# Kernel tuning notes

Hardware: AMD Instinct MI355X
Metric: run time of the kernel (lower is better)

Reference implementation:

```python
import jax, jax.numpy as jnp
import numpy as np

B, K, D = 262144, 100, 384
MOMENTUM = 0.95
EPS = 1e-8  # matches F.cosine_similarity eps clamp


def setup_inputs() -> dict:
    key = jax.random.key(0)
    k1, k2 = jax.random.split(key)
    embeddings = jax.random.normal(k1, (B, D), dtype=jnp.float32)
    centroids = jax.random.normal(k2, (K, D), dtype=jnp.float32)
    counts = jnp.zeros((K,), dtype=jnp.float32)
    return {"embeddings": embeddings, "centroids": centroids, "counts": counts}


def reference(embeddings, centroids, counts):
    # Batched version of compute_novelty: cosine similarity of each embedding
    # against every active cluster centroid (all K treated as active).
    e = embeddings / jnp.maximum(jnp.linalg.norm(embeddings, axis=-1, keepdims=True), EPS)
    c = centroids / jnp.maximum(jnp.linalg.norm(centroids, axis=-1, keepdims=True), EPS)
    sims = jnp.einsum('bd,kd->bk', e, c)            # [B, K] cosine similarities
    max_sim = jnp.max(sims, axis=-1)                # [B]
    closest = jnp.argmax(sims, axis=-1)             # [B] int
    novelty = 1.0 - max_sim * max_sim               # squared-distance novelty (FIX 4)

    # Batched EMA centroid update (update_cluster fused over the batch):
    # each cluster moves toward the mean of the embeddings assigned to it.
    num_k = centroids.shape[0]
    seg_sum = jax.ops.segment_sum(embeddings, closest, num_segments=num_k)   # [K, D]
    seg_cnt = jax.ops.segment_sum(jnp.ones((embeddings.shape[0],), embeddings.dtype),
                                  closest, num_segments=num_k)               # [K]
    seg_mean = seg_sum / jnp.maximum(seg_cnt, 1.0)[:, None]
    hit = (seg_cnt > 0)[:, None]
    new_centroids = jnp.where(hit, MOMENTUM * centroids + (1.0 - MOMENTUM) * seg_mean,
                              centroids)
    new_counts = counts + seg_cnt
    return novelty, closest, new_centroids, new_counts
```

## Files before the change

### kernel.cpp

```cpp
#include <hip/hip_runtime.h>
#include <math.h>

#define B_N 262144
#define K_N 100
#define D_N 384
#define EPS 1e-8f
#define MOM 0.95f
#define FLAG_THR 5e-4f
#define NBLK 256
#define ROWS_PB (B_N / NBLK)
#define KSTR 101
#define PART_N (K_N * D_N)

typedef __attribute__((ext_vector_type(8))) short short8;
typedef __attribute__((ext_vector_type(4))) float f32x4;

#define OFF_CPK   0
#define OFF_NC64  86016
#define OFF_CNT   86816
#define OFF_FLAGN 87264
#define OFF_FLAGS 87328
#define OFF_PARTS 1135904

#define GLOAD_LDS(g, l) __builtin_amdgcn_global_load_lds( \
    (const __attribute__((address_space(1))) unsigned int*)(g), \
    (__attribute__((address_space(3))) unsigned int*)(l), 16, 0, 0)

__device__ __forceinline__ size_t cpk_idx(int col, int d) {
    int kk = d >> 5, r = d & 31, lg = r >> 3, j = r & 7;
    int nt = col >> 4, l15 = col & 15;
    return (size_t)((kk * 7 + nt) * 512) + lg * 128 + l15 * 8 + j;
}

__device__ __forceinline__ unsigned short bf16_rne(float x) {
    unsigned u = __float_as_uint(x);
    unsigned r = (u + 0x7fff + ((u >> 16) & 1)) >> 16;
    return (unsigned short)r;
}

__global__ void k_norm_c(const float* __restrict__ c, unsigned short* __restrict__ cpk,
                         double* __restrict__ nc64, int* __restrict__ cnt,
                         int* __restrict__ flagn) {
    int col = blockIdx.x;
    int t = threadIdx.x;
    if (col == 112) {
        if (t < K_N) cnt[t] = 0;
        if (t == 0) *flagn = 0;
        return;
    }
    if (col >= K_N) {
        for (int d = t; d < D_N; d += 128) cpk[cpk_idx(col, d)] = 0;
        return;
    }
    const float* row = c + (size_t)col * D_N;
    double ss = 0.0;
    for (int d = t; d < D_N; d += 128) { double v = row[d]; ss += v * v; }
    __shared__ double red[2];
    for (int o = 32; o > 0; o >>= 1) ss += __shfl_down(ss, o);
    if ((t & 63) == 0) red[t >> 6] = ss;
    __syncthreads();
    double nc = fmax(sqrt(red[0] + red[1]), (double)EPS);
    if (t == 0) nc64[col] = nc;
    float inv = (float)(1.0 / nc);
    for (int d = t; d < D_N; d += 128)
        cpk[cpk_idx(col, d)] = bf16_rne(row[d] * inv);
}

__device__ __forceinline__ void splitA(float4 x0, float4 x1,
                                       short8& ah, short8& al, float& ss) {
    float xs[8] = {x0.x, x0.y, x0.z, x0.w, x1.x, x1.y, x1.z, x1.w};
#pragma unroll
    for (int j = 0; j < 8; j++) {
        float x = xs[j];
        unsigned xb = __float_as_uint(x);
        unsigned hb = xb & 0xffff0000u;
        float lf = x - __uint_as_float(hb);
        ah[j] = (short)(hb >> 16);
        al[j] = (short)bf16_rne(lf);
        ss = fmaf(x, x, ss);
    }
}

__global__ __launch_bounds__(512) void k_main(
    const float* __restrict__ e, const unsigned short* __restrict__ cpk,
    float* __restrict__ out_nov, float* __restrict__ out_cls,
    unsigned* __restrict__ flags, int* __restrict__ flagn) {
    __shared__ unsigned short sB[84 * 512];
    const int t = threadIdx.x;
    const int lane = t & 63;
    const int wid = t >> 6;
    const int l15 = lane & 15;
    const int lg = lane >> 4;
    const int rowbase = blockIdx.x * 128 + wid * 16;

    for (int c = wid; c < 84; c += 8)
        GLOAD_LDS((const char*)cpk + c * 1024 + lane * 16,
                  (char*)sB + c * 1024);

    const float* a0p = e + (size_t)(rowbase + l15) * D_N + lg * 8;

    float4 a[12][2];
#pragma unroll
    for (int kk = 0; kk < 12; kk++) {
        a[kk][0] = *(const float4*)(a0p + kk * 32);
        a[kk][1] = *(const float4*)(a0p + kk * 32 + 4);
    }

    f32x4 acc[7];
#pragma unroll
    for (int nt = 0; nt < 7; nt++) acc[nt] = f32x4{0.f, 0.f, 0.f, 0.f};
    float ss0 = 0.f;

    __syncthreads();

#pragma unroll
    for (int kk = 0; kk < 12; kk++) {
        short8 ah0, al0;
        splitA(a[kk][0], a[kk][1], ah0, al0, ss0);
#pragma unroll
        for (int nt = 0; nt < 7; nt++) {
            short8 bh = *(const short8*)(sB + (kk * 7 + nt) * 512 + lane * 8);
            acc[nt] = __builtin_amdgcn_mfma_f32_16x16x32_bf16(ah0, bh, acc[nt], 0, 0, 0);
            acc[nt] = __builtin_amdgcn_mfma_f32_16x16x32_bf16(al0, bh, acc[nt], 0, 0, 0);
        }
    }

    ss0 += __shfl_xor(ss0, 16); ss0 += __shfl_xor(ss0, 32);
    const int rl = lg * 4 + (l15 & 3);
    float ssr0 = __shfl(ss0, rl);

    float b0 = -3e38f, b1 = -3e38f, b2 = -3e38f, b3 = -3e38f;
    float s0 = -3e38f, s1 = -3e38f, s2 = -3e38f, s3 = -3e38f;
    int i0 = 0, i1 = 0, i2 = 0, i3 = 0, j0 = 0, j1 = 0, j2 = 0, j3 = 0;
#pragma unroll
    for (int nt = 0; nt < 7; nt++) {
        int cl = nt * 16 + l15;
        bool valid = cl < K_N;
        float v;
        v = valid ? acc[nt][0] : -3e38f;
        if (v > b0) { s0 = b0; j0 = i0; b0 = v; i0 = cl; } else if (v > s0) { s0 = v; j0 = cl; }
        v = valid ? acc[nt][1] : -3e38f;
        if (v > b1) { s1 = b1; j1 = i1; b1 = v; i1 = cl; } else if (v > s1) { s1 = v; j1 = cl; }
        v = valid ? acc[nt][2] : -3e38f;
        if (v > b2) { s2 = b2; j2 = i2; b2 = v; i2 = cl; } else if (v > s2) { s2 = v; j2 = cl; }
        v = valid ? acc[nt][3] : -3e38f;
        if (v > b3) { s3 = b3; j3 = i3; b3 = v; i3 = cl; } else if (v > s3) { s3 = v; j3 = cl; }
    }
#pragma unroll
    for (int w = 1; w <= 8; w <<= 1) {
#define MRG(B, S, I, J)                                                        \
        {                                                                      \
            float ob = __shfl_xor(B, w), os = __shfl_xor(S, w);                \
            int obi = __shfl_xor(I, w), osi = __shfl_xor(J, w);                \
            if (ob > B) {                                                      \
                float ns; int nsi;                                             \
                if (B > os) { ns = B; nsi = I; } else { ns = os; nsi = osi; }  \
                B = ob; I = obi; S = ns; J = nsi;                              \
            } else if (ob > S) { S = ob; J = obi; }                            \
        }
        MRG(b0, s0, i0, j0) MRG(b1, s1, i1, j1) MRG(b2, s2, i2, j2) MRG(b3, s3, i3, j3)
#undef MRG
    }
    if (l15 < 4) {
        float bb = (l15 & 2) ? ((l15 & 1) ? b3 : b2) : ((l15 & 1) ? b1 : b0);
        float sv = (l15 & 2) ? ((l15 & 1) ? s3 : s2) : ((l15 & 1) ? s1 : s0);
        int bi   = (l15 & 2) ? ((l15 & 1) ? i3 : i2) : ((l15 & 1) ? i1 : i0);
        int si   = (l15 & 2) ? ((l15 & 1) ? j3 : j2) : ((l15 & 1) ? j1 : j0);
        int grow = rowbase + rl;
        float nrm = fmaxf(sqrtf(ssr0), EPS);
        float msim = bb / nrm;
        out_nov[grow] = 1.f - msim * msim;
        out_cls[grow] = (float)bi;
        if (bb - sv < FLAG_THR * nrm) {
            int pos = atomicAdd(flagn, 1);
            flags[pos] = ((unsigned)grow << 14) | ((unsigned)bi << 7) | (unsigned)si;
        }
    }
}

__global__ void k_refine(const float* __restrict__ e, const float* __restrict__ c_raw,
                         const double* __restrict__ nc64, const int* __restrict__ flagn,
                         const unsigned* __restrict__ flags,
                         float* __restrict__ out_nov, float* __restrict__ out_cls) {
    int n = *flagn;
    int gw = (blockIdx.x * 256 + threadIdx.x) >> 6;
    int lane = threadIdx.x & 63;
    int nw = (gridDim.x * 256) >> 6;
    for (int i = gw; i < n; i += nw) {
        unsigned f = flags[i];
        int row = f >> 14, bi = (f >> 7) & 127, si = f & 127;
        const float* er = e + (size_t)row * D_N;
        const float* ca = c_raw + (size_t)bi * D_N;
        const float* cb = c_raw + (size_t)si * D_N;
        double d1 = 0, d2 = 0, ee = 0;
#pragma unroll
        for (int j = 0; j < 6; j++) {
            int d = lane * 6 + j;
            double ev = er[d];
            d1 += ev * (double)ca[d];
            d2 += ev * (double)cb[d];
            ee += ev * ev;
        }
#pragma unroll
        for (int w = 1; w <= 32; w <<= 1) {
            d1 += __shfl_xor(d1, w); d2 += __shfl_xor(d2, w); ee += __shfl_xor(ee, w);
        }
        if (lane == 0) {
            double v1 = d1 / nc64[bi], v2 = d2 / nc64[si];
            int k; double v;
            if (v2 > v1 || (v2 == v1 && si < bi)) { k = si; v = v2; } else { k = bi; v = v1; }
            double nrm = fmax(sqrt(ee), (double)EPS);
            double ms = v / nrm;
            out_nov[row] = (float)(1.0 - ms * ms);
            out_cls[row] = (float)k;
        }
    }
}

__global__ __launch_bounds__(768) void k_accum(
    const float* __restrict__ e, const float* __restrict__ cls,
    int* __restrict__ parts, int* __restrict__ cnt) {
    __shared__ int sums[D_N * KSTR];
    __shared__ int scls[ROWS_PB];
    __shared__ int h[K_N];
    const int t = threadIdx.x;
    const int rg = t / D_N;
    const int d = t - rg * D_N;
    const size_t rbase = (size_t)blockIdx.x * ROWS_PB;

    for (int i = t; i < D_N * KSTR; i += 768) sums[i] = 0;
    if (t < K_N) h[t] = 0;
    __syncthreads();
    for (int i = t; i < ROWS_PB; i += 768) {
        int k = (int)cls[rbase + i];
        scls[i] = k;
        atomicAdd(&h[k], 1);
    }
    __syncthreads();
    if (t < K_N && h[t] > 0) atomicAdd(&cnt[t], h[t]);

    const float* eb = e + rbase * D_N;
    for (int g = 0; g < ROWS_PB; g += 16) {
        const int r0 = g + rg,      r1 = g + rg + 2,  r2 = g + rg + 4,  r3 = g + rg + 6;
        const int r4 = g + rg + 8,  r5 = g + rg + 10, r6 = g + rg + 12, r7 = g + rg + 14;
        float v0 = eb[(size_t)r0 * D_N + d]; float v1 = eb[(size_t)r1 * D_N + d];
        float v2 = eb[(size_t)r2 * D_N + d]; float v3 = eb[(size_t)r3 * D_N + d];
        float v4 = eb[(size_t)r4 * D_N + d]; float v5 = eb[(size_t)r5 * D_N + d];
        float v6 = eb[(size_t)r6 * D_N + d]; float v7 = eb[(size_t)r7 * D_N + d];
        atomicAdd(&sums[d * KSTR + scls[r0]], __float2int_rn(v0 * 65536.f));
        atomicAdd(&sums[d * KSTR + scls[r1]], __float2int_rn(v1 * 65536.f));
        atomicAdd(&sums[d * KSTR + scls[r2]], __float2int_rn(v2 * 65536.f));
        atomicAdd(&sums[d * KSTR + scls[r3]], __float2int_rn(v3 * 65536.f));
        atomicAdd(&sums[d * KSTR + scls[r4]], __float2int_rn(v4 * 65536.f));
        atomicAdd(&sums[d * KSTR + scls[r5]], __float2int_rn(v5 * 65536.f));
        atomicAdd(&sums[d * KSTR + scls[r6]], __float2int_rn(v6 * 65536.f));
        atomicAdd(&sums[d * KSTR + scls[r7]], __float2int_rn(v7 * 65536.f));
    }
    __syncthreads();

    int* pb = parts + (size_t)blockIdx.x * PART_N;
    for (int i = t; i < PART_N; i += 768) {
        int kq = i / D_N, dr = i - kq * D_N;
        pb[i] = sums[dr * KSTR + kq];
    }
}

__global__ void k_reduce(const float* __restrict__ c_raw, const int* __restrict__ parts,
                         const int* __restrict__ cnt, const float* __restrict__ counts_in,
                         float* __restrict__ out_cent, float* __restrict__ out_cnts) {
    int idx = blockIdx.x * 256 + threadIdx.x;
    if (blockIdx.x == 0 && threadIdx.x < K_N)
        out_cnts[threadIdx.x] = counts_in[threadIdx.x] + (float)cnt[threadIdx.x];
    if (idx >= PART_N) return;
    long long s = 0;
#pragma unroll 8
    for (int b = 0; b < NBLK; b++) s += (long long)parts[(size_t)b * PART_N + idx];
    int k = idx / D_N;
    int n = cnt[k];
    float c0 = c_raw[idx];
    float mean = (float)((double)s / 65536.0 / (double)(n > 1 ? n : 1));
    out_cent[idx] = (n > 0) ? (MOM * c0 + (1.0f - MOM) * mean) : c0;
}

extern "C" void kernel_launch(void* const* d_in, const int* in_sizes, int n_in,
                              void* d_out, int out_size, void* d_ws, size_t ws_size,
                              hipStream_t stream) {
    const float* emb    = (const float*)d_in[0];
    const float* cen    = (const float*)d_in[1];
    const float* counts = (const float*)d_in[2];
    float* out = (float*)d_out;
    char* ws = (char*)d_ws;

    unsigned short* cpk   = (unsigned short*)(ws + OFF_CPK);
    double*         nc64  = (double*)(ws + OFF_NC64);
    int*            cnt   = (int*)(ws + OFF_CNT);
    int*            flagn = (int*)(ws + OFF_FLAGN);
    unsigned*       flags = (unsigned*)(ws + OFF_FLAGS);
    int*            parts = (int*)(ws + OFF_PARTS);

    float* out_nov  = out;
    float* out_cls  = out + B_N;
    float* out_cent = out + 2 * B_N;
    float* out_cnts = out + 2 * B_N + K_N * D_N;

    k_norm_c<<<113, 128, 0, stream>>>(cen, cpk, nc64, cnt, flagn);
    k_main<<<B_N / 128, 512, 0, stream>>>(emb, cpk, out_nov, out_cls, flags, flagn);
    k_refine<<<256, 256, 0, stream>>>(emb, cen, nc64, flagn, flags, out_nov, out_cls);
    k_accum<<<NBLK, 768, 0, stream>>>(emb, out_cls, parts, cnt);
    k_reduce<<<(PART_N + 255) / 256, 256, 0, stream>>>(cen, parts, cnt, counts,
                                                       out_cent, out_cnts);
}
```

Baseline: 258.2 us.

## Fuse segment accumulation into similarity kernel with refine-time corrections

Merges the similarity/argmax kernel and the segment-sum accumulation kernel into a single kernel. Each of 256 blocks processes 1024 rows and adds the register-resident embeddings into shared-memory fixed-point sums, so the embedding matrix is read from HBM once instead of twice. Rows whose assignment changes during refinement are corrected afterwards through signed 64-bit global atomics into a correction buffer and count adjustments. The cost is that the centroid tile is now read from global/L1 instead of LDS, because the LDS holds the sums. The grid also drops from 2048 blocks to 256, which lowers occupancy and latency hiding for the matmul phase.

Result: slower. 327.2 us (+26.7%).

```diff
diff --git a/kernel.cpp b/kernel.cpp
--- a/kernel.cpp
+++ b/kernel.cpp
@@ -8,7 +8,6 @@
 #define MOM 0.95f
 #define FLAG_THR 5e-4f
 #define NBLK 256
-#define ROWS_PB (B_N / NBLK)
 #define KSTR 101
 #define PART_N (K_N * D_N)
 
@@ -20,11 +19,8 @@
 #define OFF_CNT   86816
 #define OFF_FLAGN 87264
 #define OFF_FLAGS 87328
-#define OFF_PARTS 1135904
-
-#define GLOAD_LDS(g, l) __builtin_amdgcn_global_load_lds( \
-    (const __attribute__((address_space(1))) unsigned int*)(g), \
-    (__attribute__((address_space(3))) unsigned int*)(l), 16, 0, 0)
+#define OFF_CORR  1135904
+#define OFF_PARTS 1443104
 
 __device__ __forceinline__ size_t cpk_idx(int col, int d) {
     int kk = d >> 5, r = d & 31, lg = r >> 3, j = r & 7;
@@ -40,9 +36,16 @@
 
 __global__ void k_norm_c(const float* __restrict__ c, unsigned short* __restrict__ cpk,
                          double* __restrict__ nc64, int* __restrict__ cnt,
-                         int* __restrict__ flagn) {
+                         int* __restrict__ flagn, long long* __restrict__ corr) {
     int col = blockIdx.x;
     int t = threadIdx.x;
+    if (col >= 113) {
+        int base = (col - 113) * 512 + t * 4;
+#pragma unroll
+        for (int j = 0; j < 4; j++)
+            if (base + j < PART_N) corr[base + j] = 0;
+        return;
+    }
     if (col == 112) {
         if (t < K_N) cnt[t] = 0;
         if (t == 0) *flagn = 0;
@@ -81,107 +84,139 @@
     }
 }
 
-__global__ __launch_bounds__(512) void k_main(
+__global__ __launch_bounds__(512) void k_fused(
     const float* __restrict__ e, const unsigned short* __restrict__ cpk,
     float* __restrict__ out_nov, float* __restrict__ out_cls,
-    unsigned* __restrict__ flags, int* __restrict__ flagn) {
-    __shared__ unsigned short sB[84 * 512];
+    unsigned* __restrict__ flags, int* __restrict__ flagn,
+    int* __restrict__ cnt, int* __restrict__ parts) {
+    __shared__ int sums[D_N * KSTR];
+    __shared__ int hist[128];
     const int t = threadIdx.x;
     const int lane = t & 63;
     const int wid = t >> 6;
     const int l15 = lane & 15;
     const int lg = lane >> 4;
-    const int rowbase = blockIdx.x * 128 + wid * 16;
-
-    for (int c = wid; c < 84; c += 8)
-        GLOAD_LDS((const char*)cpk + c * 1024 + lane * 16,
-                  (char*)sB + c * 1024);
-
-    const float* a0p = e + (size_t)(rowbase + l15) * D_N + lg * 8;
-
-    float4 a[12][2];
-#pragma unroll
-    for (int kk = 0; kk < 12; kk++) {
-        a[kk][0] = *(const float4*)(a0p + kk * 32);
-        a[kk][1] = *(const float4*)(a0p + kk * 32 + 4);
-    }
-
-    f32x4 acc[7];
-#pragma unroll
-    for (int nt = 0; nt < 7; nt++) acc[nt] = f32x4{0.f, 0.f, 0.f, 0.f};
-    float ss0 = 0.f;
-
+
+    for (int i = t; i < D_N * KSTR; i += 512) sums[i] = 0;
+    if (t < 128) hist[t] = 0;
     __syncthreads();
 
-#pragma unroll
-    for (int kk = 0; kk < 12; kk++) {
-        short8 ah0, al0;
-        splitA(a[kk][0], a[kk][1], ah0, al0, ss0);
+    for (int ch = 0; ch < 8; ch++) {
+        __builtin_amdgcn_sched_barrier(0);
+        const int rowbase = blockIdx.x * 1024 + ch * 128 + wid * 16;
+        const float* a0p = e + (size_t)(rowbase + l15) * D_N + lg * 8;
+
+        float4 a[12][2];
+#pragma unroll
+        for (int kk = 0; kk < 12; kk++) {
+            a[kk][0] = *(const float4*)(a0p + kk * 32);
+            a[kk][1] = *(const float4*)(a0p + kk * 32 + 4);
+        }
+
+        f32x4 acc[7];
+#pragma unroll
+        for (int nt = 0; nt < 7; nt++) acc[nt] = f32x4{0.f, 0.f, 0.f, 0.f};
+        float ss0 = 0.f;
+
+#pragma unroll
+        for (int kk = 0; kk < 12; kk++) {
+            short8 ah0, al0;
+            splitA(a[kk][0], a[kk][1], ah0, al0, ss0);
+#pragma unroll
+            for (int nt = 0; nt < 7; nt++) {
+                short8 bh = *(const short8*)(cpk + (kk * 7 + nt) * 512 + lane * 8);
+                acc[nt] = __builtin_amdgcn_mfma_f32_16x16x32_bf16(ah0, bh, acc[nt], 0, 0, 0);
+                acc[nt] = __builtin_amdgcn_mfma_f32_16x16x32_bf16(al0, bh, acc[nt], 0, 0, 0);
+            }
+        }
+
+        ss0 += __shfl_xor(ss0, 16); ss0 += __shfl_xor(ss0, 32);
+        const int rl = lg * 4 + (l15 & 3);
+        float ssr0 = __shfl(ss0, rl);
+
+        float b0 = -3e38f, b1 = -3e38f, b2 = -3e38f, b3 = -3e38f;
+        float s0 = -3e38f, s1 = -3e38f, s2 = -3e38f, s3 = -3e38f;
+        int i0 = 0, i1 = 0, i2 = 0, i3 = 0, j0 = 0, j1 = 0, j2 = 0, j3 = 0;
 #pragma unroll
         for (int nt = 0; nt < 7; nt++) {
-            short8 bh = *(const short8*)(sB + (kk * 7 + nt) * 512 + lane * 8);
-            acc[nt] = __builtin_amdgcn_mfma_f32_16x16x32_bf16(ah0, bh, acc[nt], 0, 0, 0);
-            acc[nt] = __builtin_amdgcn_mfma_f32_16x16x32_bf16(al0, bh, acc[nt], 0, 0, 0);
-        }
-    }
-
-    ss0 += __shfl_xor(ss0, 16); ss0 += __shfl_xor(ss0, 32);
-    const int rl = lg * 4 + (l15 & 3);
-    float ssr0 = __shfl(ss0, rl);
-
-    float b0 = -3e38f, b1 = -3e38f, b2 = -3e38f, b3 = -3e38f;
-    float s0 = -3e38f, s1 = -3e38f, s2 = -3e38f, s3 = -3e38f;
-    int i0 = 0, i1 = 0, i2 = 0, i3 = 0, j0 = 0, j1 = 0, j2 = 0, j3 = 0;
-#pragma unroll
-    for (int nt = 0; nt < 7; nt++) {
-        int cl = nt * 16 + l15;
-        bool valid = cl < K_N;
-        float v;
-        v = valid ? acc[nt][0] : -3e38f;
-        if (v > b0) { s0 = b0; j0 = i0; b0 = v; i0 = cl; } else if (v > s0) { s0 = v; j0 = cl; }
-        v = valid ? acc[nt][1] : -3e38f;
-        if (v > b1) { s1 = b1; j1 = i1; b1 = v; i1 = cl; } else if (v > s1) { s1 = v; j1 = cl; }
-        v = valid ? acc[nt][2] : -3e38f;
-        if (v > b2) { s2 = b2; j2 = i2; b2 = v; i2 = cl; } else if (v > s2) { s2 = v; j2 = cl; }
-        v = valid ? acc[nt][3] : -3e38f;
-        if (v > b3) { s3 = b3; j3 = i3; b3 = v; i3 = cl; } else if (v > s3) { s3 = v; j3 = cl; }
-    }
-#pragma unroll
-    for (int w = 1; w <= 8; w <<= 1) {
+            int cl = nt * 16 + l15;
+            bool valid = cl < K_N;
+            float v;
+            v = valid ? acc[nt][0] : -3e38f;
+            if (v > b0) { s0 = b0; j0 = i0; b0 = v; i0 = cl; } else if (v > s0) { s0 = v; j0 = cl; }
+            v = valid ? acc[nt][1] : -3e38f;
+            if (v > b1) { s1 = b1; j1 = i1; b1 = v; i1 = cl; } else if (v > s1) { s1 = v; j1 = cl; }
+            v = valid ? acc[nt][2] : -3e38f;
+            if (v > b2) { s2 = b2; j2 = i2; b2 = v; i2 = cl; } else if (v > s2) { s2 = v; j2 = cl; }
+            v = valid ? acc[nt][3] : -3e38f;
+            if (v > b3) { s3 = b3; j3 = i3; b3 = v; i3 = cl; } else if (v > s3) { s3 = v; j3 = cl; }
+        }
+#pragma unroll
+        for (int w = 1; w <= 8; w <<= 1) {
 #define MRG(B, S, I, J)                                                        \
-        {                                                                      \
-            float ob = __shfl_xor(B, w), os = __shfl_xor(S, w);                \
-            int obi = __shfl_xor(I, w), osi = __shfl_xor(J, w);                \
-            if (ob > B) {                                                      \
-                float ns; int nsi;                                             \
-                if (B > os) { ns = B; nsi = I; } else { ns = os; nsi = osi; }  \
-                B = ob; I = obi; S = ns; J = nsi;                              \
-            } else if (ob > S) { S = ob; J = obi; }                            \
-        }
-        MRG(b0, s0, i0, j0) MRG(b1, s1, i1, j1) MRG(b2, s2, i2, j2) MRG(b3, s3, i3, j3)
+            {                                                                  \
+                float ob = __shfl_xor(B, w), os = __shfl_xor(S, w);            \
+                int obi = __shfl_xor(I, w), osi = __shfl_xor(J, w);            \
+                if (ob > B) {                                                  \
+                    float ns; int nsi;                                         \
+                    if (B > os) { ns = B; nsi = I; } else { ns = os; nsi = osi; } \
+                    B = ob; I = obi; S = ns; J = nsi;                          \
+                } else if (ob > S) { S = ob; J = obi; }                        \
+            }
+            MRG(b0, s0, i0, j0) MRG(b1, s1, i1, j1) MRG(b2, s2, i2, j2) MRG(b3, s3, i3, j3)
 #undef MRG
-    }
-    if (l15 < 4) {
-        float bb = (l15 & 2) ? ((l15 & 1) ? b3 : b2) : ((l15 & 1) ? b1 : b0);
-        float sv = (l15 & 2) ? ((l15 & 1) ? s3 : s2) : ((l15 & 1) ? s1 : s0);
-        int bi   = (l15 & 2) ? ((l15 & 1) ? i3 : i2) : ((l15 & 1) ? i1 : i0);
-        int si   = (l15 & 2) ? ((l15 & 1) ? j3 : j2) : ((l15 & 1) ? j1 : j0);
-        int grow = rowbase + rl;
-        float nrm = fmaxf(sqrtf(ssr0), EPS);
-        float msim = bb / nrm;
-        out_nov[grow] = 1.f - msim * msim;
-        out_cls[grow] = (float)bi;
-        if (bb - sv < FLAG_THR * nrm) {
-            int pos = atomicAdd(flagn, 1);
-            flags[pos] = ((unsigned)grow << 14) | ((unsigned)bi << 7) | (unsigned)si;
-        }
-    }
+        }
+        if (l15 < 4) {
+            float bb = (l15 & 2) ? ((l15 & 1) ? b3 : b2) : ((l15 & 1) ? b1 : b0);
+            float sv = (l15 & 2) ? ((l15 & 1) ? s3 : s2) : ((l15 & 1) ? s1 : s0);
+            int bi   = (l15 & 2) ? ((l15 & 1) ? i3 : i2) : ((l15 & 1) ? i1 : i0);
+            int si   = (l15 & 2) ? ((l15 & 1) ? j3 : j2) : ((l15 & 1) ? j1 : j0);
+            int grow = rowbase + rl;
+            float nrm = fmaxf(sqrtf(ssr0), EPS);
+            float msim = bb / nrm;
+            out_nov[grow] = 1.f - msim * msim;
+            out_cls[grow] = (float)bi;
+            atomicAdd(&hist[bi], 1);
+            if (bb - sv < FLAG_THR * nrm) {
+                int pos = atomicAdd(flagn, 1);
+                flags[pos] = ((unsigned)grow << 14) | ((unsigned)bi << 7) | (unsigned)si;
+            }
+        }
+
+        const int src = (l15 >> 2) * 16;
+        int k0 = __shfl(i0, src), k1 = __shfl(i1, src);
+        int k2 = __shfl(i2, src), k3 = __shfl(i3, src);
+        const int myk = (l15 & 2) ? ((l15 & 1) ? k3 : k2) : ((l15 & 1) ? k1 : k0);
+
+#pragma unroll
+        for (int kk = 0; kk < 12; kk++) {
+            int base = (kk * 32 + lg * 8) * KSTR + myk;
+            float4 v0 = a[kk][0], v1 = a[kk][1];
+            atomicAdd(&sums[base + 0 * KSTR], __float2int_rn(v0.x * 65536.f));
+            atomicAdd(&sums[base + 1 * KSTR], __float2int_rn(v0.y * 65536.f));
+            atomicAdd(&sums[base + 2 * KSTR], __float2int_rn(v0.z * 65536.f));
+            atomicAdd(&sums[base + 3 * KSTR], __float2int_rn(v0.w * 65536.f));
+            atomicAdd(&sums[base + 4 * KSTR], __float2int_rn(v1.x * 65536.f));
+            atomicAdd(&sums[base + 5 * KSTR], __float2int_rn(v1.y * 65536.f));
+            atomicAdd(&sums[base + 6 * KSTR], __float2int_rn(v1.z * 65536.f));
+            atomicAdd(&sums[base + 7 * KSTR], __float2int_rn(v1.w * 65536.f));
+        }
+    }
+
+    __syncthreads();
+    int* pb = parts + (size_t)blockIdx.x * PART_N;
+    for (int i = t; i < PART_N; i += 512) {
+        int kq = i / D_N, dr = i - kq * D_N;
+        pb[i] = sums[dr * KSTR + kq];
+    }
+    if (t < K_N && hist[t] > 0) atomicAdd(&cnt[t], hist[t]);
 }
 
 __global__ void k_refine(const float* __restrict__ e, const float* __restrict__ c_raw,
                          const double* __restrict__ nc64, const int* __restrict__ flagn,
                          const unsigned* __restrict__ flags,
-                         float* __restrict__ out_nov, float* __restrict__ out_cls) {
+                         float* __restrict__ out_nov, float* __restrict__ out_cls,
+                         int* __restrict__ cnt, unsigned long long* __restrict__ corr) {
     int n = *flagn;
     int gw = (blockIdx.x * 256 + threadIdx.x) >> 6;
     int lane = threadIdx.x & 63;
@@ -205,81 +240,46 @@
         for (int w = 1; w <= 32; w <<= 1) {
             d1 += __shfl_xor(d1, w); d2 += __shfl_xor(d2, w); ee += __shfl_xor(ee, w);
         }
+        double v1 = d1 / nc64[bi], v2 = d2 / nc64[si];
+        bool flip = (v2 > v1) || (v2 == v1 && si < bi);
+        int k = flip ? si : bi;
         if (lane == 0) {
-            double v1 = d1 / nc64[bi], v2 = d2 / nc64[si];
-            int k; double v;
-            if (v2 > v1 || (v2 == v1 && si < bi)) { k = si; v = v2; } else { k = bi; v = v1; }
+            double v = flip ? v2 : v1;
             double nrm = fmax(sqrt(ee), (double)EPS);
             double ms = v / nrm;
             out_nov[row] = (float)(1.0 - ms * ms);
             out_cls[row] = (float)k;
-        }
-    }
-}
-
-__global__ __launch_bounds__(768) void k_accum(
-    const float* __restrict__ e, const float* __restrict__ cls,
-    int* __restrict__ parts, int* __restrict__ cnt) {
-    __shared__ int sums[D_N * KSTR];
-    __shared__ int scls[ROWS_PB];
-    __shared__ int h[K_N];
-    const int t = threadIdx.x;
-    const int rg = t / D_N;
-    const int d = t - rg * D_N;
-    const size_t rbase = (size_t)blockIdx.x * ROWS_PB;
-
-    for (int i = t; i < D_N * KSTR; i += 768) sums[i] = 0;
-    if (t < K_N) h[t] = 0;
-    __syncthreads();
-    for (int i = t; i < ROWS_PB; i += 768) {
-        int k = (int)cls[rbase + i];
-        scls[i] = k;
-        atomicAdd(&h[k], 1);
-    }
-    __syncthreads();
-    if (t < K_N && h[t] > 0) atomicAdd(&cnt[t], h[t]);
-
-    const float* eb = e + rbase * D_N;
-    for (int g = 0; g < ROWS_PB; g += 16) {
-        const int r0 = g + rg,      r1 = g + rg + 2,  r2 = g + rg + 4,  r3 = g + rg + 6;
-        const int r4 = g + rg + 8,  r5 = g + rg + 10, r6 = g + rg + 12, r7 = g + rg + 14;
-        float v0 = eb[(size_t)r0 * D_N + d]; float v1 = eb[(size_t)r1 * D_N + d];
-        float v2 = eb[(size_t)r2 * D_N + d]; float v3 = eb[(size_t)r3 * D_N + d];
-        float v4 = eb[(size_t)r4 * D_N + d]; float v5 = eb[(size_t)r5 * D_N + d];
-        float v6 = eb[(size_t)r6 * D_N + d]; float v7 = eb[(size_t)r7 * D_N + d];
-        atomicAdd(&sums[d * KSTR + scls[r0]], __float2int_rn(v0 * 65536.f));
-        atomicAdd(&sums[d * KSTR + scls[r1]], __float2int_rn(v1 * 65536.f));
-        atomicAdd(&sums[d * KSTR + scls[r2]], __float2int_rn(v2 * 65536.f));
-        atomicAdd(&sums[d * KSTR + scls[r3]], __float2int_rn(v3 * 65536.f));
-        atomicAdd(&sums[d * KSTR + scls[r4]], __float2int_rn(v4 * 65536.f));
-        atomicAdd(&sums[d * KSTR + scls[r5]], __float2int_rn(v5 * 65536.f));
-        atomicAdd(&sums[d * KSTR + scls[r6]], __float2int_rn(v6 * 65536.f));
-        atomicAdd(&sums[d * KSTR + scls[r7]], __float2int_rn(v7 * 65536.f));
-    }
-    __syncthreads();
-
-    int* pb = parts + (size_t)blockIdx.x * PART_N;
-    for (int i = t; i < PART_N; i += 768) {
-        int kq = i / D_N, dr = i - kq * D_N;
-        pb[i] = sums[dr * KSTR + kq];
+            if (flip) { atomicAdd(&cnt[k], 1); atomicAdd(&cnt[bi], -1); }
+        }
+        if (flip) {
+#pragma unroll
+            for (int j = 0; j < 6; j++) {
+                int d = lane * 6 + j;
+                long long q = (long long)__float2int_rn(er[d] * 65536.f);
+                atomicAdd(&corr[k * D_N + d], (unsigned long long)q);
+                atomicAdd(&corr[bi * D_N + d], (unsigned long long)(-q));
+            }
+        }
     }
 }
 
 __global__ void k_reduce(const float* __restrict__ c_raw, const int* __restrict__ parts,
-                         const int* __restrict__ cnt, const float* __restrict__ counts_in,
+                         const long long* __restrict__ corr, const int* __restrict__ cnt,
+                         const float* __restrict__ counts_in,
                          float* __restrict__ out_cent, float* __restrict__ out_cnts) {
     int idx = blockIdx.x * 256 + threadIdx.x;
     if (blockIdx.x == 0 && threadIdx.x < K_N)
         out_cnts[threadIdx.x] = counts_in[threadIdx.x] + (float)cnt[threadIdx.x];
     if (idx >= PART_N) return;
-    long long s = 0;
+    long long s = corr[idx];
 #pragma unroll 8
     for (int b = 0; b < NBLK; b++) s += (long long)parts[(size_t)b * PART_N + idx];
     int k = idx / D_N;
+    int d = idx - k * D_N;
     int n = cnt[k];
-    float c0 = c_raw[idx];
+    float c0 = c_raw[(size_t)k * D_N + d];
     float mean = (float)((double)s / 65536.0 / (double)(n > 1 ? n : 1));
-    out_cent[idx] = (n > 0) ? (MOM * c0 + (1.0f - MOM) * mean) : c0;
+    out_cent[(size_t)k * D_N + d] = (n > 0) ? (MOM * c0 + (1.0f - MOM) * mean) : c0;
 }
 
 extern "C" void kernel_launch(void* const* d_in, const int* in_sizes, int n_in,
@@ -296,6 +296,7 @@
     int*            cnt   = (int*)(ws + OFF_CNT);
     int*            flagn = (int*)(ws + OFF_FLAGN);
     unsigned*       flags = (unsigned*)(ws + OFF_FLAGS);
+    long long*      corr  = (long long*)(ws + OFF_CORR);
     int*            parts = (int*)(ws + OFF_PARTS);
 
     float* out_nov  = out;
@@ -303,10 +304,11 @@
     float* out_cent = out + 2 * B_N;
     float* out_cnts = out + 2 * B_N + K_N * D_N;
 
-    k_norm_c<<<113, 128, 0, stream>>>(cen, cpk, nc64, cnt, flagn);
-    k_main<<<B_N / 128, 512, 0, stream>>>(emb, cpk, out_nov, out_cls, flags, flagn);
-    k_refine<<<256, 256, 0, stream>>>(emb, cen, nc64, flagn, flags, out_nov, out_cls);
-    k_accum<<<NBLK, 768, 0, stream>>>(emb, out_cls, parts, cnt);
-    k_reduce<<<(PART_N + 255) / 256, 256, 0, stream>>>(cen, parts, cnt, counts,
+    k_norm_c<<<189, 128, 0, stream>>>(cen, cpk, nc64, cnt, flagn, corr);
+    k_fused<<<NBLK, 512, 0, stream>>>(emb, cpk, out_nov, out_cls, flags, flagn,
+                                      cnt, parts);
+    k_refine<<<256, 256, 0, stream>>>(emb, cen, nc64, flagn, flags, out_nov, out_cls,
+                                      cnt, (unsigned long long*)corr);
+    k_reduce<<<(PART_N + 255) / 256, 256, 0, stream>>>(cen, parts, corr, cnt, counts,
                                                        out_cent, out_cnts);
 }
```
